# Performance work log

Measured on AMD Instinct MI355X. Metric: run time of the kernel, lower is better.

## Reference

```python
import jax, jax.numpy as jnp
import numpy as np

B, DIM = 64, 1024

def setup_inputs() -> dict:
    key = jax.random.key(0)
    ks = jax.random.split(key, 16)
    d = {
        'x': jax.random.normal(ks[0], (B, DIM), jnp.float32),
        'C': jax.random.normal(ks[1], (B, DIM, DIM), jnp.float32) * 0.02,
        'n': jax.random.normal(ks[2], (B, DIM), jnp.float32),
        'm': jax.random.normal(ks[3], (B, DIM), jnp.float32),
    }
    s = 1.0 / np.sqrt(DIM)
    names = ['q', 'k', 'v', 'i', 'f', 'o']
    for j, nm in enumerate(names):
        d['W' + nm] = jax.random.uniform(ks[4 + 2 * j], (DIM, DIM), jnp.float32, -s, s)
        d['b' + nm] = jax.random.uniform(ks[5 + 2 * j], (DIM,), jnp.float32, -s, s)
    return d

def _lin(x, W, b):
    # torch nn.Linear: x @ W.T + b
    return x @ W.T + b

def reference(x, C, n, m, Wq, bq, Wk, bk, Wv, bv, Wi, bi, Wf, bf, Wo, bo):
    q = _lin(x, Wq, bq)                      # [B, D]
    k = _lin(x, Wk, bk) / jnp.sqrt(jnp.float32(DIM))
    v = _lin(x, Wv, bv)
    i_t = _lin(x, Wi, bi)
    f_t = _lin(x, Wf, bf)
    m_new = jnp.maximum(f_t + m, i_t)        # [B, D]
    i = jnp.exp(i_t - m_new)                 # [B, D]
    f = jnp.exp(f_t + m - m_new)             # [B, D]
    # rank-1 covariance update: C_new[b,r,c] = f[b,r]*C[b,r,c] + i[b,r]*v[b,r]*k[b,c]
    C_new = f[:, :, None] * C + (i * v)[:, :, None] * k[:, None, :]
    n_new = f * n + i * k
    h = jax.nn.sigmoid(_lin(x, Wo, bo)) * jnp.einsum('brc,bc->br', C_new, q)
    return (h, C_new, n_new, m_new)
```

## Files before the change

### kernel.cpp

```cpp
#include <hip/hip_runtime.h>
#include <hip/hip_bf16.h>
#include <math.h>

#define BATCH 64
#define DIM 1024
#define NROW (BATCH * DIM)
#define OFF_H 0
#define OFF_C 65536
#define OFF_N (65536 + 67108864)
#define OFF_M (OFF_N + 65536)

typedef float f4     __attribute__((ext_vector_type(4)));
typedef float f32x4  __attribute__((ext_vector_type(4)));
typedef short bf16x8 __attribute__((ext_vector_type(8)));


__device__ inline short f2bf(float v) {
    __hip_bfloat16 h = __float2bfloat16(v);
    short s;
    __builtin_memcpy(&s, &h, 2);
    return s;
}

__device__ inline bf16x8 load_bf8(const float* __restrict__ p) {
    f4 a = *reinterpret_cast<const f4*>(p);
    f4 b = *reinterpret_cast<const f4*>(p + 4);
    bf16x8 r;
    r[0] = f2bf(a.x); r[1] = f2bf(a.y); r[2] = f2bf(a.z); r[3] = f2bf(a.w);
    r[4] = f2bf(b.x); r[5] = f2bf(b.y); r[6] = f2bf(b.z); r[7] = f2bf(b.w);
    return r;
}

__device__ inline int   biti(float f) { int i;   __builtin_memcpy(&i, &f, 4); return i; }
__device__ inline float bitf(int i)   { float f; __builtin_memcpy(&f, &i, 4); return f; }

__device__ inline float wave_sum64_dpp(float x) {
    int t;
    t = __builtin_amdgcn_update_dpp(0, biti(x), 0x111, 0xF, 0xF, true); x += bitf(t);
    t = __builtin_amdgcn_update_dpp(0, biti(x), 0x112, 0xF, 0xF, true); x += bitf(t);
    t = __builtin_amdgcn_update_dpp(0, biti(x), 0x114, 0xF, 0xF, true); x += bitf(t);
    t = __builtin_amdgcn_update_dpp(0, biti(x), 0x118, 0xF, 0xF, true); x += bitf(t);
    t = __builtin_amdgcn_update_dpp(0, biti(x), 0x142, 0xA, 0xF, true); x += bitf(t);
    t = __builtin_amdgcn_update_dpp(0, biti(x), 0x143, 0xC, 0xF, true); x += bitf(t);
    return bitf(__builtin_amdgcn_readlane(biti(x), 63));
}

__global__ __launch_bounds__(256) void gemm6_mfma(
    const float* __restrict__ x,
    const float* __restrict__ Wq, const float* __restrict__ bq,
    const float* __restrict__ Wk, const float* __restrict__ bk,
    const float* __restrict__ Wv, const float* __restrict__ bv,
    const float* __restrict__ Wi, const float* __restrict__ bi,
    const float* __restrict__ Wf, const float* __restrict__ bf_,
    const float* __restrict__ Wo, const float* __restrict__ bo,
    float* __restrict__ pre)
{
    const int bx = blockIdx.x;
    const int g  = bx >> 6;
    const int j0 = (bx & 63) << 4;
    const float* W; const float* bias;
    switch (g) {
        case 0: W = Wq; bias = bq; break;
        case 1: W = Wk; bias = bk; break;
        case 2: W = Wv; bias = bv; break;
        case 3: W = Wi; bias = bi; break;
        case 4: W = Wf; bias = bf_; break;
        default: W = Wo; bias = bo; break;
    }

    const int wave = threadIdx.x >> 6;
    const int lane = threadIdx.x & 63;
    const int l15  = lane & 15;
    const int kq   = lane >> 4;

    const float* xrow = x + (size_t)(wave * 16 + l15) * DIM + kq * 8;
    const float* wrow = W + (size_t)(j0 + l15) * DIM + kq * 8;

    f32x4 acc0 = {0.f, 0.f, 0.f, 0.f};
    f32x4 acc1 = {0.f, 0.f, 0.f, 0.f};
    #pragma unroll 4
    for (int kt = 0; kt < 32; kt += 2) {
        bf16x8 a0 = load_bf8(xrow + kt * 32);
        bf16x8 b0 = load_bf8(wrow + kt * 32);
        bf16x8 a1 = load_bf8(xrow + kt * 32 + 32);
        bf16x8 b1 = load_bf8(wrow + kt * 32 + 32);
        acc0 = __builtin_amdgcn_mfma_f32_16x16x32_bf16(a0, b0, acc0, 0, 0, 0);
        acc1 = __builtin_amdgcn_mfma_f32_16x16x32_bf16(a1, b1, acc1, 0, 0, 0);
    }
    acc0 += acc1;

    const float bv_ = bias[j0 + l15];
    float* dst = pre + (size_t)g * NROW + (size_t)(wave * 16 + kq * 4) * DIM + j0 + l15;
    #pragma unroll
    for (int r = 0; r < 4; ++r)
        dst[(size_t)r * DIM] = acc0[r] + bv_;
}

__global__ __launch_bounds__(256) void cupdate3(
    const float* __restrict__ C,
    const float* __restrict__ n_in, const float* __restrict__ m_in,
    const float* __restrict__ ws,
    float* __restrict__ out)
{
    const int row  = blockIdx.x * 4 + (threadIdx.x >> 6);
    const int lane = threadIdx.x & 63;
    const int b    = row >> 10;

    const float ip  = ws[3 * NROW + row];
    const float fp_ = ws[4 * NROW + row];
    const float op  = ws[5 * NROW + row];
    const float vp  = ws[2 * NROW + row];
    const float mo  = m_in[row];

    const float mn  = fmaxf(fp_ + mo, ip);
    const float iex = expf(ip - mn);
    const float fex = expf(fp_ + mo - mn);
    const float so  = 1.f / (1.f + expf(-op));
    const float ksc = iex * vp * 0.03125f;

    const f4* k4 = reinterpret_cast<const f4*>(ws + 1 * NROW + b * DIM);
    const f4* q4 = reinterpret_cast<const f4*>(ws + 0 * NROW + b * DIM);
    const f4* C4 = reinterpret_cast<const f4*>(C) + (size_t)row * 256;
    f4*       O4 = reinterpret_cast<f4*>(out + OFF_C) + (size_t)row * 256;

    float dotC = 0.f, dotK = 0.f;
    #pragma unroll
    for (int i = 0; i < 4; ++i) {
        const int c4 = lane + 64 * i;
        f4 cv = C4[c4];
        f4 kv = k4[c4];
        f4 qv = q4[c4];
        O4[c4] = fex * cv + ksc * kv;
        f4 pc = cv * qv;
        f4 pk = kv * qv;
        dotC += pc.x + pc.y + pc.z + pc.w;
        dotK += pk.x + pk.y + pk.z + pk.w;
    }

    const float dC = wave_sum64_dpp(dotC);
    const float dK = wave_sum64_dpp(dotK);

    if (lane == 0) {
        out[OFF_H + row] = so * (fex * dC + ksc * dK);
        out[OFF_N + row] = fex * n_in[row] + iex * ws[1 * NROW + row] * 0.03125f;
        out[OFF_M + row] = mn;
    }
}

extern "C" void kernel_launch(void* const* d_in, const int* in_sizes, int n_in,
                              void* d_out, int out_size, void* d_ws, size_t ws_size,
                              hipStream_t stream) {
    const float* x = (const float*)d_in[0];
    const float* C = (const float*)d_in[1];
    const float* n = (const float*)d_in[2];
    const float* m = (const float*)d_in[3];
    float* ws  = (float*)d_ws;
    float* out = (float*)d_out;

    gemm6_mfma<<<384, 256, 0, stream>>>(
        x,
        (const float*)d_in[4],  (const float*)d_in[5],
        (const float*)d_in[6],  (const float*)d_in[7],
        (const float*)d_in[8],  (const float*)d_in[9],
        (const float*)d_in[10], (const float*)d_in[11],
        (const float*)d_in[12], (const float*)d_in[13],
        (const float*)d_in[14], (const float*)d_in[15],
        ws);
    cupdate3<<<NROW / 4, 256, 0, stream>>>(C, n, m, ws, out);
}
```

Baseline: 132.5 us.

## Process 32 rows per block with shared k/q and hoisted k·q dot

```diff
diff --git a/kernel.cpp b/kernel.cpp
--- a/kernel.cpp
+++ b/kernel.cpp
@@ -96,54 +96,79 @@
         dst[(size_t)r * DIM] = acc0[r] + bv_;
 }
 
-__global__ __launch_bounds__(256) void cupdate3(
+#define RPB 32
+__global__ __launch_bounds__(256) void cupdate4(
     const float* __restrict__ C,
     const float* __restrict__ n_in, const float* __restrict__ m_in,
     const float* __restrict__ ws,
     float* __restrict__ out)
 {
-    const int row  = blockIdx.x * 4 + (threadIdx.x >> 6);
-    const int lane = threadIdx.x & 63;
-    const int b    = row >> 10;
+    __shared__ float kq[2][DIM];
+    __shared__ float s_fex[RPB], s_ksc[RPB], s_so[RPB];
 
-    const float ip  = ws[3 * NROW + row];
-    const float fp_ = ws[4 * NROW + row];
-    const float op  = ws[5 * NROW + row];
-    const float vp  = ws[2 * NROW + row];
-    const float mo  = m_in[row];
+    const int blk  = blockIdx.x;
+    const int b    = blk >> 5;
+    const int rg   = blk & 31;
+    const int tid  = threadIdx.x;
+    const int w    = tid >> 6;
+    const int lane = tid & 63;
 
-    const float mn  = fmaxf(fp_ + mo, ip);
-    const float iex = expf(ip - mn);
-    const float fex = expf(fp_ + mo - mn);
-    const float so  = 1.f / (1.f + expf(-op));
-    const float ksc = iex * vp * 0.03125f;
+    reinterpret_cast<f4*>(kq[0])[tid] = reinterpret_cast<const f4*>(ws + 1 * NROW + b * DIM)[tid];
+    reinterpret_cast<f4*>(kq[1])[tid] = reinterpret_cast<const f4*>(ws + 0 * NROW + b * DIM)[tid];
 
-    const f4* k4 = reinterpret_cast<const f4*>(ws + 1 * NROW + b * DIM);
-    const f4* q4 = reinterpret_cast<const f4*>(ws + 0 * NROW + b * DIM);
-    const f4* C4 = reinterpret_cast<const f4*>(C) + (size_t)row * 256;
-    f4*       O4 = reinterpret_cast<f4*>(out + OFF_C) + (size_t)row * 256;
-
-    float dotC = 0.f, dotK = 0.f;
-    #pragma unroll
-    for (int i = 0; i < 4; ++i) {
-        const int c4 = lane + 64 * i;
-        f4 cv = C4[c4];
-        f4 kv = k4[c4];
-        f4 qv = q4[c4];
-        O4[c4] = fex * cv + ksc * kv;
-        f4 pc = cv * qv;
-        f4 pk = kv * qv;
-        dotC += pc.x + pc.y + pc.z + pc.w;
-        dotK += pk.x + pk.y + pk.z + pk.w;
-    }
-
-    const float dC = wave_sum64_dpp(dotC);
-    const float dK = wave_sum64_dpp(dotK);
-
-    if (lane == 0) {
-        out[OFF_H + row] = so * (fex * dC + ksc * dK);
+    if (tid < RPB) {
+        const int row = b * DIM + rg * RPB + tid;
+        const float ip  = ws[3 * NROW + row];
+        const float fp_ = ws[4 * NROW + row];
+        const float op  = ws[5 * NROW + row];
+        const float vp  = ws[2 * NROW + row];
+        const float mo  = m_in[row];
+        const float mn  = fmaxf(fp_ + mo, ip);
+        const float iex = expf(ip - mn);
+        const float fex = expf(fp_ + mo - mn);
+        s_fex[tid] = fex;
+        s_ksc[tid] = iex * vp * 0.03125f;
+        s_so[tid]  = 1.f / (1.f + expf(-op));
         out[OFF_N + row] = fex * n_in[row] + iex * ws[1 * NROW + row] * 0.03125f;
         out[OFF_M + row] = mn;
+    }
+    __syncthreads();
+
+    const f4* kl = reinterpret_cast<const f4*>(kq[0]);
+    const f4* ql = reinterpret_cast<const f4*>(kq[1]);
+    f4 k0 = kl[lane],       k1 = kl[lane + 64],
+       k2 = kl[lane + 128], k3 = kl[lane + 192];
+    f4 q0 = ql[lane],       q1 = ql[lane + 64],
+       q2 = ql[lane + 128], q3 = ql[lane + 192];
+
+    f4 pp = k0 * q0 + k1 * q1 + k2 * q2 + k3 * q3;
+    const float kqdot = wave_sum64_dpp(pp.x + pp.y + pp.z + pp.w);
+
+    const int grow0 = b * DIM + rg * RPB + w * 8;
+    const f4* C4 = reinterpret_cast<const f4*>(C) + (size_t)grow0 * 256;
+    f4*       O4 = reinterpret_cast<f4*>(out + OFF_C) + (size_t)grow0 * 256;
+
+    #pragma unroll 2
+    for (int rr = 0; rr < 8; ++rr) {
+        const float fex = s_fex[w * 8 + rr];
+        const float ksc = s_ksc[w * 8 + rr];
+        const float so  = s_so[w * 8 + rr];
+
+        const int base = rr * 256 + lane;
+        f4 c0 = __builtin_nontemporal_load(&C4[base]);
+        f4 c1 = __builtin_nontemporal_load(&C4[base + 64]);
+        f4 c2 = __builtin_nontemporal_load(&C4[base + 128]);
+        f4 c3 = __builtin_nontemporal_load(&C4[base + 192]);
+
+        O4[base]       = fex * c0 + ksc * k0;
+        O4[base + 64]  = fex * c1 + ksc * k1;
+        O4[base + 128] = fex * c2 + ksc * k2;
+        O4[base + 192] = fex * c3 + ksc * k3;
+
+        f4 d = c0 * q0 + c1 * q1 + c2 * q2 + c3 * q3;
+        const float dC = wave_sum64_dpp(d.x + d.y + d.z + d.w);
+        if (lane == 0)
+            out[OFF_H + grow0 + rr] = so * (fex * dC + ksc * kqdot);
     }
 }
 
@@ -166,5 +191,5 @@
         (const float*)d_in[12], (const float*)d_in[13],
         (const float*)d_in[14], (const float*)d_in[15],
         ws);
-    cupdate3<<<NROW / 4, 256, 0, stream>>>(C, n, m, ws, out);
+    cupdate4<<<2048, 256, 0, stream>>>(C, n, m, ws, out);
 }
```

New measurement: 118.1 us. 10.9% less time.
